# Kernel tuning notes

Hardware: AMD Instinct MI355X
Metric: run time of the kernel (lower is better)

Reference implementation:

```python
import jax, jax.numpy as jnp
import numpy as np

KEY_CH = 256

def _conv1x1(w, b, t):
    # 1x1 conv with BN folded: t [B,Cin,N] -> [B,Cout,N]
    return jnp.einsum('oc,bcn->bon', w, t) + b[None, :, None]

def _conv1x1_relu(w, b, t):
    return jax.nn.relu(_conv1x1(w, b, t))

def setup_inputs() -> dict:
    key = jax.random.key(0)
    ks = jax.random.split(key, 12)
    B, C, H, W = 4, 512, 128, 128
    d = {}
    d['feat'] = jax.random.normal(ks[0], (B, C, H, W), jnp.float32)
    d['prob'] = jax.random.normal(ks[1], (B, 20, H, W), jnp.float32)  # unused by forward (overwritten)
    s = 0.02
    d['wp1'] = jax.random.normal(ks[2], (KEY_CH, C), jnp.float32) * s
    d['bp1'] = jnp.zeros((KEY_CH,), jnp.float32)
    d['wp2'] = jax.random.normal(ks[3], (KEY_CH, KEY_CH), jnp.float32) * s
    d['bp2'] = jnp.zeros((KEY_CH,), jnp.float32)
    d['wo1'] = jax.random.normal(ks[4], (KEY_CH, C), jnp.float32) * s
    d['bo1'] = jnp.zeros((KEY_CH,), jnp.float32)
    d['wo2'] = jax.random.normal(ks[5], (KEY_CH, KEY_CH), jnp.float32) * s
    d['bo2'] = jnp.zeros((KEY_CH,), jnp.float32)
    d['wd'] = jax.random.normal(ks[6], (KEY_CH, C), jnp.float32) * s
    d['bd'] = jnp.zeros((KEY_CH,), jnp.float32)
    d['wu'] = jax.random.normal(ks[7], (C, KEY_CH), jnp.float32) * s
    d['bu'] = jnp.zeros((C,), jnp.float32)
    d['wout'] = jax.random.normal(ks[8], (512, 2 * C), jnp.float32) * s
    d['bout'] = jnp.zeros((512,), jnp.float32)
    return d


def reference(feat, prob, wp1, bp1, wp2, bp2, wo1, bo1, wo2, bo2, wd, bd, wu, bu, wout, bout):
    B, C, H, W = feat.shape
    x = feat.reshape(B, C, H * W)  # [B,C,N]
    # prob = upsample_bilinear(feat, (H,W)) == feat (identity resize); prob arg is dead.
    # SpatialGather (scale=1): softmax over spatial, weighted pool of features.
    pw = jax.nn.softmax(x, axis=-1)                     # [B,K,N], K == C here
    context = jnp.einsum('bkn,bcn->bck', pw, x)         # [B,C,K] proxy features
    # ObjectAttentionBlock2D
    q = _conv1x1_relu(wp2, bp2, _conv1x1_relu(wp1, bp1, x))        # [B,key,N]
    k = _conv1x1_relu(wo2, bo2, _conv1x1_relu(wo1, bo1, context))  # [B,key,K]
    v = _conv1x1_relu(wd, bd, context)                             # [B,key,K]
    sim = jnp.einsum('bdn,bdk->bnk', q, k) * (KEY_CH ** -0.5)      # [B,N,K]
    sim = jax.nn.softmax(sim, axis=-1)
    ctx = jnp.einsum('bnk,bdk->bdn', sim, v)                       # [B,key,N]
    ctx = _conv1x1_relu(wu, bu, ctx)                               # [B,C,N]
    # SpatialOCR: concat + 1x1 conv + BN + ReLU (dropout identity at eval)
    out = _conv1x1_relu(wout, bout, jnp.concatenate([ctx, x], axis=1))  # [B,out,N]
    return out.reshape(B, -1, H, W)
```

## Files before the change

### kernel.cpp

```cpp
#include <hip/hip_runtime.h>

typedef unsigned int u32;
typedef unsigned short u16;
typedef short s16x8 __attribute__((ext_vector_type(8)));
typedef float f32x4 __attribute__((ext_vector_type(4)));

__device__ __forceinline__ u16 f2bf(float f) {
  u32 u = __float_as_uint(f);
  u32 r = (u + 0x7fffu + ((u >> 16) & 1u)) >> 16;
  return (u16)r;
}

template <int MODE>
__device__ __forceinline__ uint4 pack8(const float* p, float2 st) {
  float4 f0 = *(const float4*)p;
  float4 f1 = *(const float4*)(p + 4);
  float v[8] = {f0.x, f0.y, f0.z, f0.w, f1.x, f1.y, f1.z, f1.w};
  if (MODE == 2) {
#pragma unroll
    for (int j = 0; j < 8; ++j) v[j] = __expf(v[j] - st.x) * st.y;
  }
  uint4 o;
  o.x = (u32)f2bf(v[0]) | ((u32)f2bf(v[1]) << 16);
  o.y = (u32)f2bf(v[2]) | ((u32)f2bf(v[3]) << 16);
  o.z = (u32)f2bf(v[4]) | ((u32)f2bf(v[5]) << 16);
  o.w = (u32)f2bf(v[6]) | ((u32)f2bf(v[7]) << 16);
  return o;
}

__device__ __forceinline__ void g2l16(u16* lds, const u16* g) {
  __builtin_amdgcn_global_load_lds(
      (const __attribute__((address_space(1))) void*)g,
      (__attribute__((address_space(3))) void*)lds, 16, 0, 0);
}

__global__ __launch_bounds__(256) void row_softmax_bf16(
    const float* __restrict__ feat, u16* __restrict__ expx,
    u16* __restrict__ xbf) {
  const long long row = blockIdx.x;
  const float* xp = feat + row * 16384;
  const int tid = threadIdx.x, wv = tid >> 6, ln = tid & 63;
  __shared__ float red[4];
  float4 v[16];
  float mx = -1e30f;
#pragma unroll
  for (int p = 0; p < 16; ++p) {
    v[p] = *(const float4*)(xp + tid * 4 + p * 1024);
    mx = fmaxf(mx, fmaxf(fmaxf(v[p].x, v[p].y), fmaxf(v[p].z, v[p].w)));
  }
  u16* bp = xbf + row * 16384;
#pragma unroll
  for (int p = 0; p < 16; ++p) {
    uint2 ow;
    ow.x = (u32)f2bf(v[p].x) | ((u32)f2bf(v[p].y) << 16);
    ow.y = (u32)f2bf(v[p].z) | ((u32)f2bf(v[p].w) << 16);
    *(uint2*)(bp + tid * 4 + p * 1024) = ow;
  }
  for (int o = 32; o; o >>= 1) mx = fmaxf(mx, __shfl_xor(mx, o, 64));
  if (!ln) red[wv] = mx;
  __syncthreads();
  mx = fmaxf(fmaxf(red[0], red[1]), fmaxf(red[2], red[3]));
  __syncthreads();
  float s = 0.f;
#pragma unroll
  for (int p = 0; p < 16; ++p) {
    v[p].x = __expf(v[p].x - mx);
    v[p].y = __expf(v[p].y - mx);
    v[p].z = __expf(v[p].z - mx);
    v[p].w = __expf(v[p].w - mx);
    s += v[p].x + v[p].y + v[p].z + v[p].w;
  }
  for (int o = 32; o; o >>= 1) s += __shfl_xor(s, o, 64);
  if (!ln) red[wv] = s;
  __syncthreads();
  const float inv = 1.f / (red[0] + red[1] + red[2] + red[3]);
  u16* op = expx + row * 16384;
#pragma unroll
  for (int p = 0; p < 16; ++p) {
    uint2 ow;
    ow.x = (u32)f2bf(v[p].x * inv) | ((u32)f2bf(v[p].y * inv) << 16);
    ow.y = (u32)f2bf(v[p].z * inv) | ((u32)f2bf(v[p].w * inv) << 16);
    *(uint2*)(op + tid * 4 + p * 1024) = ow;
  }
}

__global__ __launch_bounds__(256) void transpose_x(const u16* __restrict__ xbf,
                                                   u16* __restrict__ catT) {
  __shared__ u16 t[32][33];
  const int b = blockIdx.z;
  const int c0 = blockIdx.y << 5, n0 = blockIdx.x << 5;
  const int tx = threadIdx.x & 31, ty = threadIdx.x >> 5;
  const u16* fb = xbf + (long long)b * 512 * 16384;
#pragma unroll
  for (int i = 0; i < 32; i += 8)
    t[ty + i][tx] = fb[(long long)(c0 + ty + i) * 16384 + n0 + tx];
  __syncthreads();
  u16* ob = catT + (long long)b * 16384 * 1024 + 512;
#pragma unroll
  for (int i = 0; i < 32; i += 8)
    ob[(long long)(n0 + ty + i) * 1024 + c0 + tx] = t[tx][ty + i];
}

__global__ __launch_bounds__(256) void cvt_weights(
    const float* __restrict__ w0, const float* __restrict__ w1,
    const float* __restrict__ w2, const float* __restrict__ w3,
    const float* __restrict__ w4, const float* __restrict__ w5,
    const float* __restrict__ w6, u16* __restrict__ dst) {
  const long long i = (long long)blockIdx.x * 256 + threadIdx.x;
  const float* s;
  long long off;
  if (i < 131072) { s = w0; off = 0; }
  else if (i < 196608) { s = w1; off = 131072; }
  else if (i < 327680) { s = w2; off = 196608; }
  else if (i < 393216) { s = w3; off = 327680; }
  else if (i < 524288) { s = w4; off = 393216; }
  else if (i < 655360) { s = w5; off = 524288; }
  else { s = w6; off = 655360; }
  dst[i] = f2bf(s[i - off]);
}

template <int ACT, int BIAS, int SPLITK, int AMODE, int BMODE, int F32OUT>
__global__ __launch_bounds__(256, 4) void gemm_nt(
    const void* __restrict__ Av, long long sA, int lda,
    const void* __restrict__ Bv, long long sB, int ldb,
    void* __restrict__ C, long long sC, int ldc,
    const float* __restrict__ bias, int K, int kchunk,
    const float2* __restrict__ stats, int statsStride) {
  __shared__ __align__(16) u16 Asm_[2][128 * 32];
  __shared__ __align__(16) u16 Bsm_[2][128 * 32];
  const int tid = threadIdx.x;
  const int wv = tid >> 6;
  const int ln = tid & 63;
  const int bz = blockIdx.z;
  const int batch = SPLITK ? (bz >> 3) : bz;
  const int chunk = SPLITK ? (bz & 7) : 0;
  const long long tm = (long long)blockIdx.y << 7;
  const long long tn = (long long)blockIdx.x << 7;
  const int lrow = ln >> 2;
  const int lcol = (((ln & 3) ^ ((ln >> 3) & 3)) << 3);
  const int w32 = wv << 5;
  const long long ar0 = tm + w32 + lrow, ar1 = ar0 + 16;
  const long long br0 = tn + w32 + lrow, br1 = br0 + 16;
  const long long koff = (long long)chunk * kchunk + lcol;
  const u16* gau0; const u16* gau1; const float* gaf0; const float* gaf1;
  if (AMODE == 0) {
    const u16* Ab = (const u16*)Av + (long long)batch * sA + koff;
    gau0 = Ab + ar0 * lda; gau1 = Ab + ar1 * lda; gaf0 = gaf1 = nullptr;
  } else {
    const float* Ab = (const float*)Av + (long long)batch * sA + koff;
    gaf0 = Ab + ar0 * lda; gaf1 = Ab + ar1 * lda; gau0 = gau1 = nullptr;
  }
  const u16* gbu0; const u16* gbu1; const float* gbf0; const float* gbf1;
  if (BMODE == 0) {
    const u16* Bb = (const u16*)Bv + (long long)batch * sB + koff;
    gbu0 = Bb + br0 * ldb; gbu1 = Bb + br1 * ldb; gbf0 = gbf1 = nullptr;
  } else {
    const float* Bb = (const float*)Bv + (long long)batch * sB + koff;
    gbf0 = Bb + br0 * ldb; gbf1 = Bb + br1 * ldb; gbu0 = gbu1 = nullptr;
  }
  float2 stA0 = make_float2(0.f, 0.f), stA1 = stA0;
  if (AMODE == 2) {
    stA0 = stats[batch * statsStride + (int)ar0];
    stA1 = stats[batch * statsStride + (int)ar1];
  }
  const int fr = ln & 15;
  const int fq = ln >> 4;
  const int wm = (wv >> 1) << 6;
  const int wn = (wv & 1) << 6;
  const int rx = (fq ^ ((fr >> 1) & 3)) << 3;
  f32x4 acc[4][4] = {};
  if (AMODE == 0 && BMODE == 0) {
    auto stage = [&](int bo, int kk) {
      g2l16(&Asm_[0][bo + w32 * 32], gau0 + kk);
      g2l16(&Asm_[0][bo + w32 * 32 + 512], gau1 + kk);
      g2l16(&Bsm_[0][bo + w32 * 32], gbu0 + kk);
      g2l16(&Bsm_[0][bo + w32 * 32 + 512], gbu1 + kk);
    };
    stage(0, 0);
    asm volatile("s_waitcnt vmcnt(0)" ::: "memory");
    asm volatile("s_barrier" ::: "memory");
    int cb = 0;
    for (int kk = 0; kk < K; kk += 32) {
      s16x8 af[4], bfr[4];
#pragma unroll
      for (int i = 0; i < 4; ++i)
        af[i] = *(const s16x8*)&Asm_[0][cb + (wm + i * 16 + fr) * 32 + rx];
#pragma unroll
      for (int j = 0; j < 4; ++j)
        bfr[j] = *(const s16x8*)&Bsm_[0][cb + (wn + j * 16 + fr) * 32 + rx];
      if (kk + 32 < K) stage(cb ^ 4096, kk + 32);
#pragma unroll
      for (int i = 0; i < 4; ++i)
#pragma unroll
        for (int j = 0; j < 4; ++j)
          acc[i][j] = __builtin_amdgcn_mfma_f32_16x16x32_bf16(
              af[i], bfr[j], acc[i][j], 0, 0, 0);
      __builtin_amdgcn_sched_barrier(0);
      asm volatile("s_waitcnt vmcnt(0) lgkmcnt(0)" ::: "memory");
      asm volatile("s_barrier" ::: "memory");
      cb ^= 4096;
    }
  } else {
    for (int kk = 0; kk < K; kk += 32) {
      uint4 ra0, ra1, rb0, rb1;
      if (AMODE == 0) {
        ra0 = *(const uint4*)(gau0 + kk);
        ra1 = *(const uint4*)(gau1 + kk);
      } else {
        ra0 = pack8<AMODE>(gaf0 + kk, stA0);
        ra1 = pack8<AMODE>(gaf1 + kk, stA1);
      }
      if (BMODE == 0) {
        rb0 = *(const uint4*)(gbu0 + kk);
        rb1 = *(const uint4*)(gbu1 + kk);
      } else {
        rb0 = pack8<BMODE>(gbf0 + kk, stA0);
        rb1 = pack8<BMODE>(gbf1 + kk, stA1);
      }
      __syncthreads();
      *(uint4*)&Asm_[0][w32 * 32 + ln * 8] = ra0;
      *(uint4*)&Asm_[0][w32 * 32 + 512 + ln * 8] = ra1;
      *(uint4*)&Bsm_[0][w32 * 32 + ln * 8] = rb0;
      *(uint4*)&Bsm_[0][w32 * 32 + 512 + ln * 8] = rb1;
      __syncthreads();
      s16x8 af[4], bfr[4];
#pragma unroll
      for (int i = 0; i < 4; ++i)
        af[i] = *(const s16x8*)&Asm_[0][(wm + i * 16 + fr) * 32 + rx];
#pragma unroll
      for (int j = 0; j < 4; ++j)
        bfr[j] = *(const s16x8*)&Bsm_[0][(wn + j * 16 + fr) * 32 + rx];
#pragma unroll
      for (int i = 0; i < 4; ++i)
#pragma unroll
        for (int j = 0; j < 4; ++j)
          acc[i][j] = __builtin_amdgcn_mfma_f32_16x16x32_bf16(
              af[i], bfr[j], acc[i][j], 0, 0, 0);
    }
  }
#pragma unroll
  for (int i = 0; i < 4; ++i) {
    const long long gr0 = tm + wm + i * 16 + fq * 4;
#pragma unroll
    for (int j = 0; j < 4; ++j) {
      const long long gc = tn + wn + j * 16 + fr;
      float bc = 0.f;
      if (BIAS == 2) bc = bias[gc];
#pragma unroll
      for (int t = 0; t < 4; ++t) {
        float v = acc[i][j][t];
        if (BIAS == 1) v += bias[gr0 + t];
        if (BIAS == 2) v += bc;
        if (ACT) v = fmaxf(v, 0.f);
        const long long idx = (long long)batch * sC + (gr0 + t) * ldc + gc;
        if (SPLITK)
          atomicAdd((float*)C + idx, v);
        else if (F32OUT)
          ((float*)C)[idx] = v;
        else
          ((u16*)C)[idx] = f2bf(v);
      }
    }
  }
}

__global__ __launch_bounds__(256) void cvt_f32_bf16(const float* __restrict__ s,
                                                    u16* __restrict__ d) {
  const int i = blockIdx.x * 256 + threadIdx.x;
  d[i] = f2bf(s[i]);
}

__global__ __launch_bounds__(256) void softmax_p(u16* __restrict__ P) {
  const int wv = threadIdx.x >> 6, ln = threadIdx.x & 63;
  const long long row = (long long)blockIdx.x * 4 + wv;
  u16* rp = P + row * 1024;
  uint4 r = *(const uint4*)(rp + ln * 8);
  u32 w[4] = {r.x, r.y, r.z, r.w};
  float v[8];
#pragma unroll
  for (int k = 0; k < 4; ++k) {
    v[2 * k] = __uint_as_float(w[k] << 16) * 0.0625f;
    v[2 * k + 1] = __uint_as_float(w[k] & 0xffff0000u) * 0.0625f;
  }
  float m = v[0];
#pragma unroll
  for (int t = 1; t < 8; ++t) m = fmaxf(m, v[t]);
  for (int o = 32; o; o >>= 1) m = fmaxf(m, __shfl_xor(m, o, 64));
  float e[8], s = 0.f;
#pragma unroll
  for (int t = 0; t < 8; ++t) {
    e[t] = __expf(v[t] - m);
    s += e[t];
  }
  for (int o = 32; o; o >>= 1) s += __shfl_xor(s, o, 64);
  const float inv = 1.f / s;
  u32 ow[4];
#pragma unroll
  for (int k = 0; k < 4; ++k)
    ow[k] = (u32)f2bf(e[2 * k] * inv) | ((u32)f2bf(e[2 * k + 1] * inv) << 16);
  *(uint4*)(rp + ln * 8) = make_uint4(ow[0], ow[1], ow[2], ow[3]);
}

extern "C" void kernel_launch(void* const* d_in, const int* in_sizes, int n_in,
                              void* d_out, int out_size, void* d_ws, size_t ws_size,
                              hipStream_t stream) {
  const float* feat = (const float*)d_in[0];
  const float* wp1 = (const float*)d_in[2];
  const float* bp1 = (const float*)d_in[3];
  const float* wp2 = (const float*)d_in[4];
  const float* bp2 = (const float*)d_in[5];
  const float* wo1 = (const float*)d_in[6];
  const float* bo1 = (const float*)d_in[7];
  const float* wo2 = (const float*)d_in[8];
  const float* bo2 = (const float*)d_in[9];
  const float* wd = (const float*)d_in[10];
  const float* bd = (const float*)d_in[11];
  const float* wu = (const float*)d_in[12];
  const float* bu = (const float*)d_in[13];
  const float* wout = (const float*)d_in[14];
  const float* bout = (const float*)d_in[15];
  float* outp = (float*)d_out;
  char* ws = (char*)d_ws;

  u16* catT = (u16*)ws;
  u16* expx = (u16*)(ws + 134217728LL);
  u16* q1T = (u16*)(ws + 134217728LL);
  u16* ctxT = q1T;
  u16* qT = (u16*)(ws + 167772160LL);
  float* ctxF = (float*)(ws + 201326592LL);
  u16* wb = (u16*)(ws + 201326592LL);
  u16* conT = (u16*)(ws + 205520896LL);
  u16* k1hT = (u16*)(ws + 207618048LL);
  u16* kTm = (u16*)(ws + 208666624LL);
  u16* vm = (u16*)(ws + 209715200LL);
  if (ws_size < 210763776ULL) return;
  u16* xbf = (u16*)d_out;
  u16* wp1b = wb + 0;
  u16* wp2b = wb + 131072;
  u16* wo1b = wb + 196608;
  u16* wo2b = wb + 327680;
  u16* wdb = wb + 393216;
  u16* wub = wb + 524288;
  u16* woutb = wb + 655360;

  row_softmax_bf16<<<2048, 256, 0, stream>>>(feat, expx, xbf);
  transpose_x<<<dim3(512, 16, 4), 256, 0, stream>>>(xbf, catT);
  hipMemsetAsync(ctxF, 0, 4194304, stream);
  gemm_nt<0, 0, 1, 0, 0, 0><<<dim3(4, 4, 32), 256, 0, stream>>>(
      expx, 8388608LL, 16384, xbf, 8388608LL, 16384, ctxF, 262144LL, 512,
      nullptr, 2048, 2048, nullptr, 0);
  cvt_f32_bf16<<<4096, 256, 0, stream>>>(ctxF, conT);
  cvt_weights<<<4608, 256, 0, stream>>>(wp1, wp2, wo1, wo2, wd, wu, wout, wb);
  gemm_nt<1, 2, 0, 0, 0, 0><<<dim3(2, 4, 4), 256, 0, stream>>>(
      conT, 262144LL, 512, wo1b, 0LL, 512, k1hT, 131072LL, 256, bo1, 512, 0,
      nullptr, 0);
  gemm_nt<1, 2, 0, 0, 0, 0><<<dim3(2, 4, 4), 256, 0, stream>>>(
      k1hT, 131072LL, 256, wo2b, 0LL, 256, kTm, 131072LL, 256, bo2, 256, 0,
      nullptr, 0);
  gemm_nt<1, 1, 0, 0, 0, 0><<<dim3(4, 2, 4), 256, 0, stream>>>(
      wdb, 0LL, 512, conT, 262144LL, 512, vm, 131072LL, 512, bd, 512, 0,
      nullptr, 0);
  gemm_nt<1, 2, 0, 0, 0, 0><<<dim3(2, 128, 4), 256, 0, stream>>>(
      catT + 512, 16777216LL, 1024, wp1b, 0LL, 512, q1T, 4194304LL, 256, bp1,
      512, 0, nullptr, 0);
  gemm_nt<1, 2, 0, 0, 0, 0><<<dim3(2, 128, 4), 256, 0, stream>>>(
      q1T, 4194304LL, 256, wp2b, 0LL, 256, qT, 4194304LL, 256, bp2, 256, 0,
      nullptr, 0);
  gemm_nt<0, 0, 0, 0, 0, 0><<<dim3(4, 128, 4), 256, 0, stream>>>(
      qT, 4194304LL, 256, kTm, 131072LL, 256, catT, 16777216LL, 1024, nullptr,
      256, 0, nullptr, 0);
  softmax_p<<<16384, 256, 0, stream>>>(catT);
  gemm_nt<0, 0, 0, 0, 0, 0><<<dim3(2, 128, 4), 256, 0, stream>>>(
      catT, 16777216LL, 1024, vm, 131072LL, 512, ctxT, 4194304LL, 256, nullptr,
      512, 0, nullptr, 0);
  gemm_nt<1, 2, 0, 0, 0, 0><<<dim3(4, 128, 4), 256, 0, stream>>>(
      ctxT, 4194304LL, 256, wub, 0LL, 256, catT, 16777216LL, 1024, bu, 256, 0,
      nullptr, 0);
  gemm_nt<1, 1, 0, 0, 0, 1><<<dim3(128, 4, 4), 256, 0, stream>>>(
      woutb, 0LL, 1024, catT, 16777216LL, 1024, outp, 8388608LL, 16384, bout,
      1024, 0, nullptr, 0);
}
```

Before: 676.6 us.

## Add 256x256-tile 512-thread GEMM kernel and route large GEMMs through it

```diff
diff --git a/kernel.cpp b/kernel.cpp
--- a/kernel.cpp
+++ b/kernel.cpp
@@ -117,6 +117,113 @@
   else if (i < 655360) { s = w5; off = 524288; }
   else { s = w6; off = 655360; }
   dst[i] = f2bf(s[i - off]);
+}
+
+template <int ACT, int BIAS, int SPLITK, int F32OUT>
+__global__ __launch_bounds__(512, 1) void gemm256_nt(
+    const u16* __restrict__ A, long long sA, int lda,
+    const u16* __restrict__ B, long long sB, int ldb,
+    void* __restrict__ C, long long sC, int ldc,
+    const float* __restrict__ bias, int K, int kchunk) {
+  __shared__ __align__(16) u16 As[2][256 * 64];
+  __shared__ __align__(16) u16 Bs[2][256 * 64];
+  const int tid = threadIdx.x;
+  const int wid = tid >> 6, ln = tid & 63;
+  const int bz = blockIdx.z;
+  const int batch = SPLITK ? (bz >> SPLITK) : bz;
+  const int chunk = SPLITK ? (bz & ((1 << SPLITK) - 1)) : 0;
+  const long long tm = (long long)blockIdx.y << 8;
+  const long long tn = (long long)blockIdx.x << 8;
+  const int srow = wid * 8 + (ln >> 3);
+  const int scl = ((ln & 7) ^ (ln >> 3)) << 3;
+  const long long koff = SPLITK ? (long long)chunk * kchunk : 0;
+  const u16* Ab = A + (long long)batch * sA + koff + scl;
+  const u16* Bb = B + (long long)batch * sB + koff + scl;
+  const u16* rA[4];
+  const u16* rB[4];
+#pragma unroll
+  for (int s = 0; s < 4; ++s) {
+    rA[s] = Ab + (tm + s * 64 + srow) * (long long)lda;
+    rB[s] = Bb + (tn + s * 64 + srow) * (long long)ldb;
+  }
+  auto stage = [&](int buf, int kk) {
+#pragma unroll
+    for (int s = 0; s < 4; ++s) {
+      g2l16(&As[buf][s * 4096 + wid * 512], rA[s] + kk);
+      g2l16(&Bs[buf][s * 4096 + wid * 512], rB[s] + kk);
+    }
+  };
+  const int fr = ln & 15, fq = ln >> 4;
+  const int wm8 = wid >> 2;
+  const int wn8 = wid & 3;
+  const int arow = (wm8 * 128 + fr) * 64;
+  const int brow = (wn8 * 64 + fr) * 64;
+  const int ax = fr & 7;
+  const int c0 = ((fq ^ ax) << 3);
+  const int c1 = c0 ^ 32;
+  f32x4 acc[8][4] = {};
+  const int nt = (SPLITK ? kchunk : K) >> 6;
+  stage(0, 0);
+  asm volatile("s_waitcnt vmcnt(0)" ::: "memory");
+  asm volatile("s_barrier" ::: "memory");
+  for (int t = 0; t < nt; ++t) {
+    const int cur = t & 1;
+    if (t + 1 < nt) stage(cur ^ 1, (t + 1) << 6);
+    s16x8 bfr[4][2];
+#pragma unroll
+    for (int nf = 0; nf < 4; ++nf) {
+      bfr[nf][0] = *(const s16x8*)&Bs[cur][brow + nf * 1024 + c0];
+      bfr[nf][1] = *(const s16x8*)&Bs[cur][brow + nf * 1024 + c1];
+    }
+#pragma unroll
+    for (int ph = 0; ph < 4; ++ph) {
+      s16x8 a0k0 = *(const s16x8*)&As[cur][arow + (2 * ph) * 1024 + c0];
+      s16x8 a0k1 = *(const s16x8*)&As[cur][arow + (2 * ph) * 1024 + c1];
+      s16x8 a1k0 = *(const s16x8*)&As[cur][arow + (2 * ph + 1) * 1024 + c0];
+      s16x8 a1k1 = *(const s16x8*)&As[cur][arow + (2 * ph + 1) * 1024 + c1];
+      __builtin_amdgcn_s_setprio(1);
+#pragma unroll
+      for (int nf = 0; nf < 4; ++nf) {
+        acc[2 * ph][nf] = __builtin_amdgcn_mfma_f32_16x16x32_bf16(
+            a0k0, bfr[nf][0], acc[2 * ph][nf], 0, 0, 0);
+        acc[2 * ph][nf] = __builtin_amdgcn_mfma_f32_16x16x32_bf16(
+            a0k1, bfr[nf][1], acc[2 * ph][nf], 0, 0, 0);
+        acc[2 * ph + 1][nf] = __builtin_amdgcn_mfma_f32_16x16x32_bf16(
+            a1k0, bfr[nf][0], acc[2 * ph + 1][nf], 0, 0, 0);
+        acc[2 * ph + 1][nf] = __builtin_amdgcn_mfma_f32_16x16x32_bf16(
+            a1k1, bfr[nf][1], acc[2 * ph + 1][nf], 0, 0, 0);
+      }
+      __builtin_amdgcn_s_setprio(0);
+    }
+    if (t + 1 < nt) {
+      asm volatile("s_waitcnt vmcnt(0)" ::: "memory");
+      asm volatile("s_barrier" ::: "memory");
+    }
+  }
+#pragma unroll
+  for (int mf = 0; mf < 8; ++mf) {
+    const long long gr0 = tm + wm8 * 128 + mf * 16 + fq * 4;
+#pragma unroll
+    for (int nf = 0; nf < 4; ++nf) {
+      const long long gc = tn + wn8 * 64 + nf * 16 + fr;
+      float bc = 0.f;
+      if (BIAS == 2) bc = bias[gc];
+#pragma unroll
+      for (int t = 0; t < 4; ++t) {
+        float v = acc[mf][nf][t];
+        if (BIAS == 1) v += bias[gr0 + t];
+        if (BIAS == 2) v += bc;
+        if (ACT) v = fmaxf(v, 0.f);
+        const long long idx = (long long)batch * sC + (gr0 + t) * ldc + gc;
+        if (SPLITK)
+          atomicAdd((float*)C + idx, v);
+        else if (F32OUT)
+          ((float*)C)[idx] = v;
+        else
+          ((u16*)C)[idx] = f2bf(v);
+      }
+    }
+  }
 }
 
 template <int ACT, int BIAS, int SPLITK, int AMODE, int BMODE, int F32OUT>
@@ -142,101 +249,45 @@
   const long long ar0 = tm + w32 + lrow, ar1 = ar0 + 16;
   const long long br0 = tn + w32 + lrow, br1 = br0 + 16;
   const long long koff = (long long)chunk * kchunk + lcol;
-  const u16* gau0; const u16* gau1; const float* gaf0; const float* gaf1;
-  if (AMODE == 0) {
-    const u16* Ab = (const u16*)Av + (long long)batch * sA + koff;
-    gau0 = Ab + ar0 * lda; gau1 = Ab + ar1 * lda; gaf0 = gaf1 = nullptr;
-  } else {
-    const float* Ab = (const float*)Av + (long long)batch * sA + koff;
-    gaf0 = Ab + ar0 * lda; gaf1 = Ab + ar1 * lda; gau0 = gau1 = nullptr;
-  }
-  const u16* gbu0; const u16* gbu1; const float* gbf0; const float* gbf1;
-  if (BMODE == 0) {
-    const u16* Bb = (const u16*)Bv + (long long)batch * sB + koff;
-    gbu0 = Bb + br0 * ldb; gbu1 = Bb + br1 * ldb; gbf0 = gbf1 = nullptr;
-  } else {
-    const float* Bb = (const float*)Bv + (long long)batch * sB + koff;
-    gbf0 = Bb + br0 * ldb; gbf1 = Bb + br1 * ldb; gbu0 = gbu1 = nullptr;
-  }
-  float2 stA0 = make_float2(0.f, 0.f), stA1 = stA0;
-  if (AMODE == 2) {
-    stA0 = stats[batch * statsStride + (int)ar0];
-    stA1 = stats[batch * statsStride + (int)ar1];
-  }
+  const u16* gau0 = (const u16*)Av + (long long)batch * sA + koff + ar0 * lda;
+  const u16* gau1 = (const u16*)Av + (long long)batch * sA + koff + ar1 * lda;
+  const u16* gbu0 = (const u16*)Bv + (long long)batch * sB + koff + br0 * ldb;
+  const u16* gbu1 = (const u16*)Bv + (long long)batch * sB + koff + br1 * ldb;
   const int fr = ln & 15;
   const int fq = ln >> 4;
   const int wm = (wv >> 1) << 6;
   const int wn = (wv & 1) << 6;
   const int rx = (fq ^ ((fr >> 1) & 3)) << 3;
   f32x4 acc[4][4] = {};
-  if (AMODE == 0 && BMODE == 0) {
-    auto stage = [&](int bo, int kk) {
-      g2l16(&Asm_[0][bo + w32 * 32], gau0 + kk);
-      g2l16(&Asm_[0][bo + w32 * 32 + 512], gau1 + kk);
-      g2l16(&Bsm_[0][bo + w32 * 32], gbu0 + kk);
-      g2l16(&Bsm_[0][bo + w32 * 32 + 512], gbu1 + kk);
-    };
-    stage(0, 0);
-    asm volatile("s_waitcnt vmcnt(0)" ::: "memory");
+  auto stage = [&](int bo, int kk) {
+    g2l16(&Asm_[0][bo + w32 * 32], gau0 + kk);
+    g2l16(&Asm_[0][bo + w32 * 32 + 512], gau1 + kk);
+    g2l16(&Bsm_[0][bo + w32 * 32], gbu0 + kk);
+    g2l16(&Bsm_[0][bo + w32 * 32 + 512], gbu1 + kk);
+  };
+  stage(0, 0);
+  asm volatile("s_waitcnt vmcnt(0)" ::: "memory");
+  asm volatile("s_barrier" ::: "memory");
+  int cb = 0;
+  for (int kk = 0; kk < K; kk += 32) {
+    s16x8 af[4], bfr[4];
+#pragma unroll
+    for (int i = 0; i < 4; ++i)
+      af[i] = *(const s16x8*)&Asm_[0][cb + (wm + i * 16 + fr) * 32 + rx];
+#pragma unroll
+    for (int j = 0; j < 4; ++j)
+      bfr[j] = *(const s16x8*)&Bsm_[0][cb + (wn + j * 16 + fr) * 32 + rx];
+    if (kk + 32 < K) stage(cb ^ 4096, kk + 32);
+#pragma unroll
+    for (int i = 0; i < 4; ++i)
+#pragma unroll
+      for (int j = 0; j < 4; ++j)
+        acc[i][j] = __builtin_amdgcn_mfma_f32_16x16x32_bf16(
+            af[i], bfr[j], acc[i][j], 0, 0, 0);
+    __builtin_amdgcn_sched_barrier(0);
+    asm volatile("s_waitcnt vmcnt(0) lgkmcnt(0)" ::: "memory");
     asm volatile("s_barrier" ::: "memory");
-    int cb = 0;
-    for (int kk = 0; kk < K; kk += 32) {
-      s16x8 af[4], bfr[4];
-#pragma unroll
-      for (int i = 0; i < 4; ++i)
-        af[i] = *(const s16x8*)&Asm_[0][cb + (wm + i * 16 + fr) * 32 + rx];
-#pragma unroll
-      for (int j = 0; j < 4; ++j)
-        bfr[j] = *(const s16x8*)&Bsm_[0][cb + (wn + j * 16 + fr) * 32 + rx];
-      if (kk + 32 < K) stage(cb ^ 4096, kk + 32);
-#pragma unroll
-      for (int i = 0; i < 4; ++i)
-#pragma unroll
-        for (int j = 0; j < 4; ++j)
-          acc[i][j] = __builtin_amdgcn_mfma_f32_16x16x32_bf16(
-              af[i], bfr[j], acc[i][j], 0, 0, 0);
-      __builtin_amdgcn_sched_barrier(0);
-      asm volatile("s_waitcnt vmcnt(0) lgkmcnt(0)" ::: "memory");
-      asm volatile("s_barrier" ::: "memory");
-      cb ^= 4096;
-    }
-  } else {
-    for (int kk = 0; kk < K; kk += 32) {
-      uint4 ra0, ra1, rb0, rb1;
-      if (AMODE == 0) {
-        ra0 = *(const uint4*)(gau0 + kk);
-        ra1 = *(const uint4*)(gau1 + kk);
-      } else {
-        ra0 = pack8<AMODE>(gaf0 + kk, stA0);
-        ra1 = pack8<AMODE>(gaf1 + kk, stA1);
-      }
-      if (BMODE == 0) {
-        rb0 = *(const uint4*)(gbu0 + kk);
-        rb1 = *(const uint4*)(gbu1 + kk);
-      } else {
-        rb0 = pack8<BMODE>(gbf0 + kk, stA0);
-        rb1 = pack8<BMODE>(gbf1 + kk, stA1);
-      }
-      __syncthreads();
-      *(uint4*)&Asm_[0][w32 * 32 + ln * 8] = ra0;
-      *(uint4*)&Asm_[0][w32 * 32 + 512 + ln * 8] = ra1;
-      *(uint4*)&Bsm_[0][w32 * 32 + ln * 8] = rb0;
-      *(uint4*)&Bsm_[0][w32 * 32 + 512 + ln * 8] = rb1;
-      __syncthreads();
-      s16x8 af[4], bfr[4];
-#pragma unroll
-      for (int i = 0; i < 4; ++i)
-        af[i] = *(const s16x8*)&Asm_[0][(wm + i * 16 + fr) * 32 + rx];
-#pragma unroll
-      for (int j = 0; j < 4; ++j)
-        bfr[j] = *(const s16x8*)&Bsm_[0][(wn + j * 16 + fr) * 32 + rx];
-#pragma unroll
-      for (int i = 0; i < 4; ++i)
-#pragma unroll
-        for (int j = 0; j < 4; ++j)
-          acc[i][j] = __builtin_amdgcn_mfma_f32_16x16x32_bf16(
-              af[i], bfr[j], acc[i][j], 0, 0, 0);
-    }
+    cb ^= 4096;
   }
 #pragma unroll
   for (int i = 0; i < 4; ++i) {
@@ -346,9 +397,9 @@
   row_softmax_bf16<<<2048, 256, 0, stream>>>(feat, expx, xbf);
   transpose_x<<<dim3(512, 16, 4), 256, 0, stream>>>(xbf, catT);
   hipMemsetAsync(ctxF, 0, 4194304, stream);
-  gemm_nt<0, 0, 1, 0, 0, 0><<<dim3(4, 4, 32), 256, 0, stream>>>(
+  gemm256_nt<0, 0, 4, 0><<<dim3(2, 2, 64), 512, 0, stream>>>(
       expx, 8388608LL, 16384, xbf, 8388608LL, 16384, ctxF, 262144LL, 512,
-      nullptr, 2048, 2048, nullptr, 0);
+      nullptr, 16384, 1024);
   cvt_f32_bf16<<<4096, 256, 0, stream>>>(ctxF, conT);
   cvt_weights<<<4608, 256, 0, stream>>>(wp1, wp2, wo1, wo2, wd, wu, wout, wb);
   gemm_nt<1, 2, 0, 0, 0, 0><<<dim3(2, 4, 4), 256, 0, stream>>>(
@@ -360,23 +411,21 @@
   gemm_nt<1, 1, 0, 0, 0, 0><<<dim3(4, 2, 4), 256, 0, stream>>>(
       wdb, 0LL, 512, conT, 262144LL, 512, vm, 131072LL, 512, bd, 512, 0,
       nullptr, 0);
-  gemm_nt<1, 2, 0, 0, 0, 0><<<dim3(2, 128, 4), 256, 0, stream>>>(
+  gemm256_nt<1, 2, 0, 0><<<dim3(1, 64, 4), 512, 0, stream>>>(
       catT + 512, 16777216LL, 1024, wp1b, 0LL, 512, q1T, 4194304LL, 256, bp1,
-      512, 0, nullptr, 0);
-  gemm_nt<1, 2, 0, 0, 0, 0><<<dim3(2, 128, 4), 256, 0, stream>>>(
-      q1T, 4194304LL, 256, wp2b, 0LL, 256, qT, 4194304LL, 256, bp2, 256, 0,
-      nullptr, 0);
-  gemm_nt<0, 0, 0, 0, 0, 0><<<dim3(4, 128, 4), 256, 0, stream>>>(
+      512, 0);
+  gemm256_nt<1, 2, 0, 0><<<dim3(1, 64, 4), 512, 0, stream>>>(
+      q1T, 4194304LL, 256, wp2b, 0LL, 256, qT, 4194304LL, 256, bp2, 256, 0);
+  gemm256_nt<0, 0, 0, 0><<<dim3(2, 64, 4), 512, 0, stream>>>(
       qT, 4194304LL, 256, kTm, 131072LL, 256, catT, 16777216LL, 1024, nullptr,
-      256, 0, nullptr, 0);
+      256, 0);
   softmax_p<<<16384, 256, 0, stream>>>(catT);
-  gemm_nt<0, 0, 0, 0, 0, 0><<<dim3(2, 128, 4), 256, 0, stream>>>(
+  gemm256_nt<0, 0, 0, 0><<<dim3(1, 64, 4), 512, 0, stream>>>(
       catT, 16777216LL, 1024, vm, 131072LL, 512, ctxT, 4194304LL, 256, nullptr,
-      512, 0, nullptr, 0);
-  gemm_nt<1, 2, 0, 0, 0, 0><<<dim3(4, 128, 4), 256, 0, stream>>>(
-      ctxT, 4194304LL, 256, wub, 0LL, 256, catT, 16777216LL, 1024, bu, 256, 0,
-      nullptr, 0);
-  gemm_nt<1, 1, 0, 0, 0, 1><<<dim3(128, 4, 4), 256, 0, stream>>>(
+      512, 0);
+  gemm256_nt<1, 2, 0, 0><<<dim3(2, 64, 4), 512, 0, stream>>>(
+      ctxT, 4194304LL, 256, wub, 0LL, 256, catT, 16777216LL, 1024, bu, 256, 0);
+  gemm256_nt<1, 1, 0, 1><<<dim3(64, 2, 4), 512, 0, stream>>>(
       woutb, 0LL, 1024, catT, 16777216LL, 1024, outp, 8388608LL, 16384, bout,
-      1024, 0, nullptr, 0);
-}
+      1024, 0);
+}
```

After: 669.0 us. About the same (-1.1%).
